# Performance work log

Hardware: AMD Instinct MI355X
Metric: run time of the kernel (lower is better)

The kernel has to match this reference:

```python
import jax, jax.numpy as jnp
import numpy as np

B, T, D = 2, 1024, 1024
H, HKV = 16, 8
HD = D // H           # 64
NREP = H // HKV       # 2
NLAYERS = 3
MAXKV = T * NLAYERS   # 3072
EPS = 1e-5


def setup_inputs() -> dict:
    key = jax.random.key(0)
    ks = jax.random.split(key, 8)
    # rotary tables over full accumulated-KV range
    inv_freq = 1.0 / (10000.0 ** (jnp.arange(0, HD, 2, dtype=jnp.float32) / HD))  # (HD/2,)
    t = jnp.arange(MAXKV, dtype=jnp.float32)
    freqs = jnp.outer(t, inv_freq)  # (MAXKV, HD/2)
    return {
        "x": jax.random.normal(ks[0], (B, T, D), jnp.float32),
        "cos": jnp.cos(freqs),
        "sin": jnp.sin(freqs),
        "q_w": jax.random.normal(ks[1], (NLAYERS, D, D), jnp.float32) * 0.02,
        "k_w": jax.random.normal(ks[2], (NLAYERS, D // NREP, D), jnp.float32) * 0.02,
        "v_w": jax.random.normal(ks[3], (NLAYERS, D // NREP, D), jnp.float32) * 0.02,
        "ln_w": jnp.ones((NLAYERS, D), jnp.float32),
        "lam": jax.random.normal(ks[4], (NLAYERS,), jnp.float32) * 0.1,
        "out_w": jax.random.normal(ks[5], (D, D), jnp.float32) * 0.02,
        "final_ln_w": jnp.ones((D,), jnp.float32),
        "alpha": jnp.ones((1,), jnp.float32),
    }


def rmsnorm(x, w):
    return x * jax.lax.rsqrt(jnp.mean(x * x, axis=-1, keepdims=True) + EPS) * w


def rope(x, cos, sin):
    # x: (B, L, h, HD); cos/sin: (MAXKV, HD/2); flash_attn non-interleaved rotary
    L = x.shape[1]
    c = jnp.concatenate([cos[:L], cos[:L]], axis=-1)[None, :, None, :]
    s = jnp.concatenate([sin[:L], sin[:L]], axis=-1)[None, :, None, :]
    x1, x2 = jnp.split(x, 2, axis=-1)
    rot = jnp.concatenate([-x2, x1], axis=-1)
    return x * c + rot * s


def reference(x, cos, sin, q_w, k_w, v_w, ln_w, lam, out_w, final_ln_w, alpha):
    scale = HD ** -0.5
    # lambda weights: layernorm over sigmoid of the 3 scalars (biased var, eps=1e-5)
    s = jax.nn.sigmoid(lam)
    lw = (s - s.mean()) * jax.lax.rsqrt(s.var() + EPS)
    qidx = jnp.arange(T)
    k_list, v_list = [], []
    acc = jnp.zeros_like(x)
    for i in range(NLAYERS):
        q = (x @ q_w[i].T).reshape(B, T, H, HD)
        k = (x @ k_w[i].T).reshape(B, T, HKV, HD)
        v = (x @ v_w[i].T).reshape(B, T, HKV, HD)
        k_list.append(k)
        v_list.append(v)
        K = jnp.concatenate(k_list, axis=1)  # (B, L, HKV, HD), L=(i+1)*T
        V = jnp.concatenate(v_list, axis=1)
        L = K.shape[1]
        qr = rope(q, cos, sin)
        Kr = rope(K, cos, sin)  # whole buffer re-rotated each layer, as in original
        Kr = jnp.repeat(Kr, NREP, axis=2)  # GQA expand
        Vr = jnp.repeat(V, NREP, axis=2)
        scores = jnp.einsum('bqhd,bkhd->bhqk', qr, Kr) * scale
        # flash_attn causal=True with kv_len > q_len aligns bottom-right
        mask = jnp.arange(L)[None, :] <= (qidx + (L - T))[:, None]
        scores = jnp.where(mask[None, None], scores, -jnp.inf)
        attn = jax.nn.softmax(scores, axis=-1)
        o = jnp.einsum('bhqk,bkhd->bqhd', attn, Vr).reshape(B, T, D)
        acc = acc + rmsnorm(o, ln_w[i]) * lw[i]
    out = rmsnorm(acc + alpha * x, final_ln_w)
    return out @ out_w.T
```

## Files before the change

### kernel.cpp

```cpp
#include <hip/hip_runtime.h>
#include <type_traits>
#include <utility>

typedef unsigned short u16;
typedef unsigned int u32;
typedef short short8 __attribute__((ext_vector_type(8)));
typedef __bf16 bf16x8 __attribute__((ext_vector_type(8)));
typedef float floatx4 __attribute__((ext_vector_type(4)));

template <typename V, typename = void> struct MfmaTakes : std::false_type {};
template <typename V>
struct MfmaTakes<V, std::void_t<decltype(__builtin_amdgcn_mfma_f32_16x16x32_bf16(
    std::declval<V>(), std::declval<V>(), std::declval<floatx4>(), 0, 0, 0))>>
    : std::true_type {};

template <typename V>
__device__ __forceinline__ floatx4 mfma_impl(V a, V b, floatx4 c, std::true_type) {
  return __builtin_amdgcn_mfma_f32_16x16x32_bf16(a, b, c, 0, 0, 0);
}
template <typename V>
__device__ __forceinline__ floatx4 mfma_impl(V a, V b, floatx4 c, std::false_type) {
  return __builtin_amdgcn_mfma_f32_16x16x32_bf16(
      __builtin_bit_cast(bf16x8, a), __builtin_bit_cast(bf16x8, b), c, 0, 0, 0);
}
__device__ __forceinline__ floatx4 MFMA16(short8 a, short8 b, floatx4 c) {
  return mfma_impl<short8>(a, b, c, MfmaTakes<short8>{});
}

__device__ __forceinline__ u16 f2bf(float f) {
  union { float f; unsigned u; } x; x.f = f;
  unsigned r = (x.u + 0x7fffu + ((x.u >> 16) & 1u)) >> 16;
  return (u16)r;
}
__device__ __forceinline__ float bf2f(u16 v) {
  union { unsigned u; float f; } x; x.u = ((unsigned)v) << 16; return x.f;
}
__device__ __forceinline__ u32 packbf(float lo, float hi) {
  return (__float_as_uint(hi) & 0xffff0000u) | (__float_as_uint(lo) >> 16);
}
__device__ __forceinline__ u32 pack2bf(float lo, float hi) {
  return ((u32)f2bf(hi) << 16) | (u32)f2bf(lo);
}

#if defined(__has_builtin)
#if __has_builtin(__builtin_amdgcn_global_load_lds)
#define HAS_GLLDS 1
#endif
#endif
__device__ __forceinline__ void stage16(const u16* g, u16* lbase, int lane) {
#ifdef HAS_GLLDS
  __builtin_amdgcn_global_load_lds(
      (__attribute__((address_space(1))) void*)(g),
      (__attribute__((address_space(3))) void*)(lbase), 16, 0, 0);
#else
  *(uint4*)(lbase + lane * 8) = *(const uint4*)g;
#endif
}

__global__ __launch_bounds__(256) void prep_kernel(
    const float* __restrict__ x, const float* __restrict__ qw,
    const float* __restrict__ kw, const float* __restrict__ vw,
    const float* __restrict__ outw, const float* __restrict__ lam,
    u16* __restrict__ xb, u16* __restrict__ wcat, u16* __restrict__ outwb,
    float* __restrict__ lwbuf) {
  size_t gid = (size_t)blockIdx.x * 256 + threadIdx.x;
  if (gid == 0) {
    float s0 = 1.f / (1.f + expf(-lam[0]));
    float s1 = 1.f / (1.f + expf(-lam[1]));
    float s2 = 1.f / (1.f + expf(-lam[2]));
    float mean = (s0 + s1 + s2) * (1.f / 3.f);
    float d0 = s0 - mean, d1 = s1 - mean, d2 = s2 - mean;
    float var = (d0 * d0 + d1 * d1 + d2 * d2) * (1.f / 3.f);
    float r = rsqrtf(var + 1e-5f);
    lwbuf[0] = d0 * r; lwbuf[1] = d1 * r; lwbuf[2] = d2 * r;
  }
  if (gid < 524288) {
    float4 v = ((const float4*)x)[gid];
    ushort4 o; o.x = f2bf(v.x); o.y = f2bf(v.y); o.z = f2bf(v.z); o.w = f2bf(v.w);
    ((ushort4*)xb)[gid] = o;
    return;
  }
  size_t g2 = gid - 524288;
  if (g2 < 1572864) {
    int col4 = (int)(g2 & 255);
    int n = (int)(g2 >> 8);
    int layer = n >> 11, r = n & 2047;
    const float* srcrow;
    if (r < 1024) srcrow = qw + ((size_t)(layer * 1024 + r) << 10);
    else if (r < 1536) srcrow = kw + ((size_t)(layer * 512 + (r - 1024)) << 10);
    else srcrow = vw + ((size_t)(layer * 512 + (r - 1536)) << 10);
    float4 v = ((const float4*)srcrow)[col4];
    ushort4 o; o.x = f2bf(v.x); o.y = f2bf(v.y); o.z = f2bf(v.z); o.w = f2bf(v.w);
    ((ushort4*)wcat)[g2] = o;
    return;
  }
  size_t g3 = g2 - 1572864;
  if (g3 < 262144) {
    float4 v = ((const float4*)outw)[g3];
    ushort4 o; o.x = f2bf(v.x); o.y = f2bf(v.y); o.z = f2bf(v.z); o.w = f2bf(v.w);
    ((ushort4*)outwb)[g3] = o;
  }
}

__global__ __launch_bounds__(256) void gemm_qkv(
    const u16* __restrict__ A, const u16* __restrict__ Bw,
    const float* __restrict__ cosb, const float* __restrict__ sinb,
    u16* __restrict__ qr, u16* __restrict__ kr, u16* __restrict__ vt) {
  __shared__ u16 As[128][64];
  __shared__ u16 Bs[128][64];
  const unsigned flat = blockIdx.x;
  const int bm = (flat >> 3) & 15;
  const int bn = ((flat >> 7) << 3) + (flat & 7);
  const int tid = threadIdx.x;
  const int wave = tid >> 6, lane = tid & 63;
  const int quad = lane >> 4, l16 = lane & 15;
  const int wm = wave & 1, wn = wave >> 1;
  const int srow = lane >> 3, skc = (lane & 7) * 8;
  floatx4 acc[4][4];
#pragma unroll
  for (int i = 0; i < 4; i++)
#pragma unroll
    for (int j = 0; j < 4; j++) { acc[i][j][0] = 0.f; acc[i][j][1] = 0.f; acc[i][j][2] = 0.f; acc[i][j][3] = 0.f; }
  const u16* Abase = A + (size_t)(bm * 128) * 1024;
  const u16* Bbase = Bw + (size_t)(bn * 128) * 1024;
  for (int k0 = 0; k0 < 1024; k0 += 64) {
    __syncthreads();
#pragma unroll
    for (int i = 0; i < 4; i++) {
      int ch = wave * 4 + i;
      stage16(Abase + (size_t)(ch * 8 + srow) * 1024 + k0 + skc, &As[ch * 8][0], lane);
      stage16(Bbase + (size_t)(ch * 8 + srow) * 1024 + k0 + skc, &Bs[ch * 8][0], lane);
    }
    __syncthreads();
#pragma unroll
    for (int kf = 0; kf < 2; kf++) {
      short8 af[4], bf[4];
#pragma unroll
      for (int mi = 0; mi < 4; mi++)
        af[mi] = *(const short8*)(&As[wm * 64 + mi * 16 + l16][kf * 32 + quad * 8]);
#pragma unroll
      for (int ni = 0; ni < 4; ni++)
        bf[ni] = *(const short8*)(&Bs[wn * 64 + ni * 16 + l16][kf * 32 + quad * 8]);
#pragma unroll
      for (int mi = 0; mi < 4; mi++)
#pragma unroll
        for (int ni = 0; ni < 4; ni++)
          acc[mi][ni] = MFMA16(af[mi], bf[ni], acc[mi][ni]);
    }
  }
  const int f0 = bn * 128 + wn * 64;
  const int lay = f0 >> 11;
  const int r0 = f0 & 2047;
  const int mrow0 = bm * 128 + wm * 64;
  if (r0 < 1024) {
    const int h = r0 >> 6;
#pragma unroll
    for (int mi = 0; mi < 4; mi++)
#pragma unroll
      for (int rr = 0; rr < 4; rr++) {
        int m = mrow0 + mi * 16 + quad * 4 + rr;
        int b = m >> 10, t = m & 1023;
        const float* cp = cosb + (size_t)t * 32;
        const float* sp = sinb + (size_t)t * 32;
        float c0 = cp[l16], s0 = sp[l16];
        float c1 = cp[16 + l16], s1 = sp[16 + l16];
        float x10 = acc[mi][0][rr], x20 = acc[mi][2][rr];
        float x11 = acc[mi][1][rr], x21 = acc[mi][3][rr];
        u16* row = qr + ((((size_t)lay * 2 + b) * 16 + h) * 1024 + t) * 64;
        row[l16]      = f2bf((x10 * c0 - x20 * s0) * 0.125f);
        row[16 + l16] = f2bf((x11 * c1 - x21 * s1) * 0.125f);
        row[32 + l16] = f2bf((x20 * c0 + x10 * s0) * 0.125f);
        row[48 + l16] = f2bf((x21 * c1 + x11 * s1) * 0.125f);
      }
  } else if (r0 < 1536) {
    const int hk = (r0 - 1024) >> 6;
#pragma unroll
    for (int mi = 0; mi < 4; mi++)
#pragma unroll
      for (int rr = 0; rr < 4; rr++) {
        int m = mrow0 + mi * 16 + quad * 4 + rr;
        int b = m >> 10, t = m & 1023;
        int pos = lay * 1024 + t;
        const float* cp = cosb + (size_t)pos * 32;
        const float* sp = sinb + (size_t)pos * 32;
        float c0 = cp[l16], s0 = sp[l16];
        float c1 = cp[16 + l16], s1 = sp[16 + l16];
        float x10 = acc[mi][0][rr], x20 = acc[mi][2][rr];
        float x11 = acc[mi][1][rr], x21 = acc[mi][3][rr];
        u16* row = kr + (((size_t)(b * 8 + hk)) * 3072 + pos) * 64;
        row[l16]      = f2bf(x10 * c0 - x20 * s0);
        row[16 + l16] = f2bf(x11 * c1 - x21 * s1);
        row[32 + l16] = f2bf(x20 * c0 + x10 * s0);
        row[48 + l16] = f2bf(x21 * c1 + x11 * s1);
      }
  } else {
    const int hv = (r0 - 1536) >> 6;
#pragma unroll
    for (int mi = 0; mi < 4; mi++) {
      int m0 = mrow0 + mi * 16 + quad * 4;
      int b = m0 >> 10;
      int pos0 = lay * 1024 + (m0 & 1023);
      u16* colbase = vt + ((size_t)(b * 8 + hv) * 64) * 3072 + pos0;
#pragma unroll
      for (int ni = 0; ni < 4; ni++) {
        int d = ni * 16 + l16;
        uint2 st;
        st.x = pack2bf(acc[mi][ni][0], acc[mi][ni][1]);
        st.y = pack2bf(acc[mi][ni][2], acc[mi][ni][3]);
        *(uint2*)(colbase + (size_t)d * 3072) = st;
      }
    }
  }
}

__global__ __launch_bounds__(256) void gemm_bt(
    const u16* __restrict__ A, const u16* __restrict__ Bw,
    float* __restrict__ C, int N, int K) {
  __shared__ u16 As[64][72];
  __shared__ u16 Bs[64][72];
  const int bm = blockIdx.x, bn = blockIdx.y;
  const int tid = threadIdx.x;
  const int wave = tid >> 6, lane = tid & 63;
  const int quad = lane >> 4, l16 = lane & 15;
  const int lr = tid >> 2, lc = (tid & 3) << 4;
  floatx4 acc[4];
#pragma unroll
  for (int i = 0; i < 4; i++) { acc[i][0] = 0.f; acc[i][1] = 0.f; acc[i][2] = 0.f; acc[i][3] = 0.f; }
  const u16* Arow = A + (size_t)(bm * 64 + lr) * K;
  const u16* Brow = Bw + (size_t)(bn * 64 + lr) * K;
  for (int k0 = 0; k0 < K; k0 += 64) {
    __syncthreads();
    *(uint4*)(&As[lr][lc])     = *(const uint4*)(Arow + k0 + lc);
    *(uint4*)(&As[lr][lc + 8]) = *(const uint4*)(Arow + k0 + lc + 8);
    *(uint4*)(&Bs[lr][lc])     = *(const uint4*)(Brow + k0 + lc);
    *(uint4*)(&Bs[lr][lc + 8]) = *(const uint4*)(Brow + k0 + lc + 8);
    __syncthreads();
    const int mrow = wave * 16 + l16;
    short8 a0 = *(const short8*)(&As[mrow][quad * 8]);
    short8 a1 = *(const short8*)(&As[mrow][32 + quad * 8]);
#pragma unroll
    for (int ns = 0; ns < 4; ns++) {
      short8 b0 = *(const short8*)(&Bs[ns * 16 + l16][quad * 8]);
      short8 b1 = *(const short8*)(&Bs[ns * 16 + l16][32 + quad * 8]);
      acc[ns] = MFMA16(a0, b0, acc[ns]);
      acc[ns] = MFMA16(a1, b1, acc[ns]);
    }
  }
#pragma unroll
  for (int ns = 0; ns < 4; ns++)
#pragma unroll
    for (int r = 0; r < 4; r++) {
      int row = bm * 64 + wave * 16 + quad * 4 + r;
      int col = bn * 64 + ns * 16 + l16;
      C[(size_t)row * N + col] = acc[ns][r];
    }
}

__global__ __launch_bounds__(256) void attn_v5(
    const u16* __restrict__ qr, const u16* __restrict__ kr,
    const u16* __restrict__ vt, u16* __restrict__ obS,
    float* __restrict__ lbufp) {
  __shared__ u16 Kt[32][72];
  __shared__ u16 Vtt[64][40];
  __shared__ u16 Pw[4][16][40];
  const unsigned flat = blockIdx.x;
  const int bhz = (int)((flat >> 6) * 8 + (flat & 7));
  const int qtile = 7 - (int)((flat >> 3) & 7);
  const int z = bhz >> 5;
  const int bh = bhz & 31;
  const int lay = (z == 5) ? 0 : ((z == 0 || z == 4) ? 1 : 2);
  const int n = lay * 32 + qtile * 4 + 4;
  int kt0, kt1;
  if (lay == 0) { kt0 = 0; kt1 = n; }
  else if (lay == 1) { int hf = n >> 1; kt0 = (z == 0) ? 0 : hf; kt1 = (z == 0) ? hf : n; }
  else {
    int t1 = n / 3, t2 = (2 * n) / 3;
    kt0 = (z == 1) ? 0 : ((z == 2) ? t1 : t2);
    kt1 = (z == 1) ? t1 : ((z == 2) ? t2 : n);
  }
  const int maskkt = lay * 32 + qtile * 4;
  const int b = bh >> 4, h = bh & 15, hk = h >> 1;
  const int tid = threadIdx.x, wave = tid >> 6, lane = tid & 63;
  const int quad = lane >> 4, l16 = lane & 15;
  const int qeffbase = lay * 1024 + qtile * 128 + wave * 32;
  const u16* qpb = qr + ((((size_t)lay * 2 + b) * 16 + h) * 1024
                         + qtile * 128 + wave * 32 + l16) * 64 + quad * 8;
  short8 qf[2][2];
  qf[0][0] = *(const short8*)(qpb);
  qf[0][1] = *(const short8*)(qpb + 32);
  qf[1][0] = *(const short8*)(qpb + 1024);
  qf[1][1] = *(const short8*)(qpb + 1056);
  const short8 ones = {16256, 16256, 16256, 16256, 16256, 16256, 16256, 16256};
  floatx4 oacc[2][4];
#pragma unroll
  for (int nt = 0; nt < 2; nt++)
#pragma unroll
    for (int dt = 0; dt < 4; dt++) { oacc[nt][dt][0] = 0.f; oacc[nt][dt][1] = 0.f; oacc[nt][dt][2] = 0.f; oacc[nt][dt][3] = 0.f; }
  floatx4 lacc[2];
  lacc[0][0] = 0.f; lacc[0][1] = 0.f; lacc[0][2] = 0.f; lacc[0][3] = 0.f;
  lacc[1] = lacc[0];
  const int ksr = tid >> 3, ksc = (tid & 7) * 8;
  const int vdr = tid >> 2, vdc = (tid & 3) * 8;
  const u16* kp = kr + ((size_t)(b * 8 + hk) * 3072 + kt0 * 32 + ksr) * 64 + ksc;
  const u16* vp = vt + ((size_t)(b * 8 + hk) * 64 + vdr) * 3072 + kt0 * 32 + vdc;
  uint4 kA = *(const uint4*)kp;
  uint4 vA = *(const uint4*)vp;
  for (int kt = kt0; kt < kt1; kt++) {
    kp += 2048; vp += 32;
    __syncthreads();
    *(uint4*)(&Kt[ksr][ksc])  = kA;
    *(uint4*)(&Vtt[vdr][vdc]) = vA;
    if (kt + 1 < kt1) { kA = *(const uint4*)kp; vA = *(const uint4*)vp; }
    __syncthreads();
    const bool needmask = (kt >= maskkt);
    uint2 pk[2][2];
#pragma unroll
    for (int mt = 0; mt < 2; mt++) {
      short8 kfa = *(const short8*)(&Kt[mt * 16 + l16][quad * 8]);
      short8 kfb = *(const short8*)(&Kt[mt * 16 + l16][32 + quad * 8]);
      const int keyb = kt * 32 + mt * 16 + quad * 4;
#pragma unroll
      for (int nt = 0; nt < 2; nt++) {
        floatx4 s; s[0] = 0.f; s[1] = 0.f; s[2] = 0.f; s[3] = 0.f;
        s = MFMA16(kfa, qf[nt][0], s);
        s = MFMA16(kfb, qf[nt][1], s);
        float p0 = __expf(s[0]), p1 = __expf(s[1]);
        float p2 = __expf(s[2]), p3 = __expf(s[3]);
        if (needmask) {
          int qpos = qeffbase + nt * 16 + l16;
          if (keyb + 0 > qpos) p0 = 0.f;
          if (keyb + 1 > qpos) p1 = 0.f;
          if (keyb + 2 > qpos) p2 = 0.f;
          if (keyb + 3 > qpos) p3 = 0.f;
        }
        pk[mt][nt].x = packbf(p0, p1);
        pk[mt][nt].y = packbf(p2, p3);
      }
    }
    short8 vf[4];
#pragma unroll
    for (int dt = 0; dt < 4; dt++)
      vf[dt] = *(const short8*)(&Vtt[dt * 16 + l16][quad * 8]);
#pragma unroll
    for (int nt = 0; nt < 2; nt++) {
      *(uint2*)(&Pw[wave][l16][quad * 4])      = pk[0][nt];
      *(uint2*)(&Pw[wave][l16][16 + quad * 4]) = pk[1][nt];
      short8 pf = *(const short8*)(&Pw[wave][l16][quad * 8]);
      lacc[nt] = MFMA16(ones, pf, lacc[nt]);
#pragma unroll
      for (int dt = 0; dt < 4; dt++)
        oacc[nt][dt] = MFMA16(vf[dt], pf, oacc[nt][dt]);
    }
  }
  float* Pf = (float*)(&Pw[wave][0][0]);
  const int tt = lane >> 2, dd = (lane & 3) << 2;
#pragma unroll
  for (int nt = 0; nt < 2; nt++) {
    int t = qtile * 128 + wave * 32 + nt * 16 + l16;
    if (quad == 0)
      lbufp[((size_t)z * 2048 + b * 1024 + t) * 16 + h] = lacc[nt][0];
    int t2 = qtile * 128 + wave * 32 + nt * 16 + tt;
    u16* orow = obS + ((size_t)(z * 2 + b) * 1024 + t2) * 1024 + h * 64 + dd;
#pragma unroll
    for (int dt = 0; dt < 4; dt++) {
      *(floatx4*)(&Pf[l16 * 20 + quad * 4]) = oacc[nt][dt];
      floatx4 val = *(const floatx4*)(&Pf[tt * 20 + dd]);
      uint2 st; st.x = pack2bf(val[0], val[1]); st.y = pack2bf(val[2], val[3]);
      *(uint2*)(orow + dt * 16) = st;
    }
  }
}

__device__ __forceinline__ float block_sum(float v, float* red) {
  v += __shfl_xor(v, 32); v += __shfl_xor(v, 16); v += __shfl_xor(v, 8);
  v += __shfl_xor(v, 4);  v += __shfl_xor(v, 2);  v += __shfl_xor(v, 1);
  __syncthreads();
  if ((threadIdx.x & 63) == 0) red[threadIdx.x >> 6] = v;
  __syncthreads();
  return red[0] + red[1] + red[2] + red[3];
}

__global__ __launch_bounds__(256) void fused_norm(
    const u16* __restrict__ obS, const float* __restrict__ lbufp,
    const float* __restrict__ x, const float* __restrict__ lnw,
    const float* __restrict__ lwbuf, const float* __restrict__ flnw,
    const float* __restrict__ alphap, u16* __restrict__ y) {
  __shared__ float red[4];
  const int row = blockIdx.x, tid = threadIdx.x;
  float a[4] = {0.f, 0.f, 0.f, 0.f};
  const int nsl[3] = {1, 2, 3};
  const int sl[3][3] = {{5, 0, 0}, {0, 4, 0}, {1, 2, 3}};
#pragma unroll
  for (int l = 0; l < 3; l++) {
    float o0 = 0.f, o1 = 0.f, o2 = 0.f, o3 = 0.f, ls = 0.f;
#pragma unroll
    for (int si = 0; si < 3; si++) {
      if (si >= nsl[l]) break;
      int z = sl[l][si];
      uint2 v = ((const uint2*)(obS + ((size_t)z * 2048 + row) * 1024))[tid];
      o0 += bf2f((u16)(v.x & 0xffff)); o1 += bf2f((u16)(v.x >> 16));
      o2 += bf2f((u16)(v.y & 0xffff)); o3 += bf2f((u16)(v.y >> 16));
      ls += lbufp[((size_t)z * 2048 + row) * 16 + (tid >> 4)];
    }
    float linv = 1.f / ls;
    float v0 = o0 * linv, v1 = o1 * linv, v2 = o2 * linv, v3 = o3 * linv;
    float ss = v0 * v0 + v1 * v1 + v2 * v2 + v3 * v3;
    ss = block_sum(ss, red);
    float rstd = rsqrtf(ss * (1.f / 1024.f) + 1e-5f);
    float lw = lwbuf[l];
    float4 w = ((const float4*)(lnw + (size_t)l * 1024))[tid];
    a[0] += v0 * rstd * w.x * lw;
    a[1] += v1 * rstd * w.y * lw;
    a[2] += v2 * rstd * w.z * lw;
    a[3] += v3 * rstd * w.w * lw;
  }
  const float aa = alphap[0];
  float4 xv = ((const float4*)(x + (size_t)row * 1024))[tid];
  float v0 = a[0] + aa * xv.x, v1 = a[1] + aa * xv.y;
  float v2 = a[2] + aa * xv.z, v3 = a[3] + aa * xv.w;
  float ss = v0 * v0 + v1 * v1 + v2 * v2 + v3 * v3;
  ss = block_sum(ss, red);
  float rstd = rsqrtf(ss * (1.f / 1024.f) + 1e-5f);
  float4 fw = ((const float4*)flnw)[tid];
  ushort4 o;
  o.x = f2bf(v0 * rstd * fw.x); o.y = f2bf(v1 * rstd * fw.y);
  o.z = f2bf(v2 * rstd * fw.z); o.w = f2bf(v3 * rstd * fw.w);
  ((ushort4*)(y + (size_t)row * 1024))[tid] = o;
}

extern "C" void kernel_launch(void* const* d_in, const int* in_sizes, int n_in,
                              void* d_out, int out_size, void* d_ws, size_t ws_size,
                              hipStream_t stream) {
  const float* x     = (const float*)d_in[0];
  const float* cosb  = (const float*)d_in[1];
  const float* sinb  = (const float*)d_in[2];
  const float* qw    = (const float*)d_in[3];
  const float* kw    = (const float*)d_in[4];
  const float* vw    = (const float*)d_in[5];
  const float* lnw   = (const float*)d_in[6];
  const float* lam   = (const float*)d_in[7];
  const float* outw  = (const float*)d_in[8];
  const float* flnw  = (const float*)d_in[9];
  const float* alphap= (const float*)d_in[10];
  float* out = (float*)d_out;
  char* ws = (char*)d_ws;
  u16*   xb    = (u16*)  (ws + 0);
  u16*   wcat  = (u16*)  (ws + 4194304);
  u16*   obS   = (u16*)  (ws + 0);
  u16*   outwb = (u16*)  (ws + 25165824);
  float* lwbuf = (float*)(ws + 27262976);
  u16*   qr    = (u16*)  (ws + 27264000);
  u16*   kr    = (u16*)  (ws + 39846912);
  u16*   vt    = (u16*)  (ws + 46138368);
  float* lbufp = (float*)(ws + 52429824);
  u16*   yb    = (u16*)  (ws + 53216256);

  prep_kernel<<<9216, 256, 0, stream>>>(x, qw, kw, vw, outw, lam, xb, wcat, outwb, lwbuf);
  gemm_qkv<<<768, 256, 0, stream>>>(xb, wcat, cosb, sinb, qr, kr, vt);
  attn_v5<<<1536, 256, 0, stream>>>(qr, kr, vt, obS, lbufp);
  fused_norm<<<2048, 256, 0, stream>>>(obS, lbufp, x, lnw, lwbuf, flnw, alphap, yb);
  gemm_bt<<<dim3(32, 16), 256, 0, stream>>>(yb, outwb, out, 1024, 1024);
}
```

Before: 253.9 us.

## Double-buffer attention K/V tiles, keep P in registers via 16x16x16 MFMA, use exp2

The attention kernel now double-buffers the K and V shared-memory tiles, which removes one of the two barriers per key tile. The P matrix no longer round-trips through shared memory; it feeds 16x16x16 bf16 MFMAs straight from registers. Q is prescaled by log2(e)/8 so the softmax exponent can use the hardware exp2. In exchange, the narrower MFMA needs twice as many instructions for PV and the row-sum, and shared-memory use for K/V doubles.

```diff
diff --git a/kernel.cpp b/kernel.cpp
--- a/kernel.cpp
+++ b/kernel.cpp
@@ -5,6 +5,7 @@
 typedef unsigned short u16;
 typedef unsigned int u32;
 typedef short short8 __attribute__((ext_vector_type(8)));
+typedef short s16x4 __attribute__((ext_vector_type(4)));
 typedef __bf16 bf16x8 __attribute__((ext_vector_type(8)));
 typedef float floatx4 __attribute__((ext_vector_type(4)));
 
@@ -26,6 +27,20 @@
 __device__ __forceinline__ floatx4 MFMA16(short8 a, short8 b, floatx4 c) {
   return mfma_impl<short8>(a, b, c, MfmaTakes<short8>{});
 }
+
+__device__ __forceinline__ floatx4 MFMAK16(s16x4 a, s16x4 b, floatx4 c) {
+  return __builtin_amdgcn_mfma_f32_16x16x16bf16_1k(a, b, c, 0, 0, 0);
+}
+
+#if defined(__has_builtin)
+#if __has_builtin(__builtin_amdgcn_exp2f)
+#define EXP2(x) __builtin_amdgcn_exp2f(x)
+#else
+#define EXP2(x) exp2f(x)
+#endif
+#else
+#define EXP2(x) exp2f(x)
+#endif
 
 __device__ __forceinline__ u16 f2bf(float f) {
   union { float f; unsigned u; } x; x.f = f;
@@ -56,6 +71,8 @@
   *(uint4*)(lbase + lane * 8) = *(const uint4*)g;
 #endif
 }
+
+#define QSCALE 0.18033688011112042f
 
 __global__ __launch_bounds__(256) void prep_kernel(
     const float* __restrict__ x, const float* __restrict__ qw,
@@ -167,10 +184,10 @@
         float x10 = acc[mi][0][rr], x20 = acc[mi][2][rr];
         float x11 = acc[mi][1][rr], x21 = acc[mi][3][rr];
         u16* row = qr + ((((size_t)lay * 2 + b) * 16 + h) * 1024 + t) * 64;
-        row[l16]      = f2bf((x10 * c0 - x20 * s0) * 0.125f);
-        row[16 + l16] = f2bf((x11 * c1 - x21 * s1) * 0.125f);
-        row[32 + l16] = f2bf((x20 * c0 + x10 * s0) * 0.125f);
-        row[48 + l16] = f2bf((x21 * c1 + x11 * s1) * 0.125f);
+        row[l16]      = f2bf((x10 * c0 - x20 * s0) * QSCALE);
+        row[16 + l16] = f2bf((x11 * c1 - x21 * s1) * QSCALE);
+        row[32 + l16] = f2bf((x20 * c0 + x10 * s0) * QSCALE);
+        row[48 + l16] = f2bf((x21 * c1 + x11 * s1) * QSCALE);
       }
   } else if (r0 < 1536) {
     const int hk = (r0 - 1024) >> 6;
@@ -256,13 +273,13 @@
     }
 }
 
-__global__ __launch_bounds__(256) void attn_v5(
+__global__ __launch_bounds__(256) void attn_v6(
     const u16* __restrict__ qr, const u16* __restrict__ kr,
     const u16* __restrict__ vt, u16* __restrict__ obS,
     float* __restrict__ lbufp) {
-  __shared__ u16 Kt[32][72];
-  __shared__ u16 Vtt[64][40];
-  __shared__ u16 Pw[4][16][40];
+  __shared__ __align__(16) u16 Kt[2][32][72];
+  __shared__ __align__(16) u16 Vtt[2][64][40];
+  __shared__ __align__(16) u16 Pw[4][16][40];
   const unsigned flat = blockIdx.x;
   const int bhz = (int)((flat >> 6) * 8 + (flat & 7));
   const int qtile = 7 - (int)((flat >> 3) & 7);
@@ -290,7 +307,7 @@
   qf[0][1] = *(const short8*)(qpb + 32);
   qf[1][0] = *(const short8*)(qpb + 1024);
   qf[1][1] = *(const short8*)(qpb + 1056);
-  const short8 ones = {16256, 16256, 16256, 16256, 16256, 16256, 16256, 16256};
+  const s16x4 ones4 = {16256, 16256, 16256, 16256};
   floatx4 oacc[2][4];
 #pragma unroll
   for (int nt = 0; nt < 2; nt++)
@@ -305,27 +322,33 @@
   const u16* vp = vt + ((size_t)(b * 8 + hk) * 64 + vdr) * 3072 + kt0 * 32 + vdc;
   uint4 kA = *(const uint4*)kp;
   uint4 vA = *(const uint4*)vp;
+  *(uint4*)(&Kt[0][ksr][ksc])  = kA;
+  *(uint4*)(&Vtt[0][vdr][vdc]) = vA;
+  kp += 2048; vp += 32;
+  if (kt0 + 1 < kt1) { kA = *(const uint4*)kp; vA = *(const uint4*)vp; }
   for (int kt = kt0; kt < kt1; kt++) {
-    kp += 2048; vp += 32;
+    const int p = (kt - kt0) & 1;
     __syncthreads();
-    *(uint4*)(&Kt[ksr][ksc])  = kA;
-    *(uint4*)(&Vtt[vdr][vdc]) = vA;
-    if (kt + 1 < kt1) { kA = *(const uint4*)kp; vA = *(const uint4*)vp; }
-    __syncthreads();
+    if (kt + 1 < kt1) {
+      *(uint4*)(&Kt[p ^ 1][ksr][ksc])  = kA;
+      *(uint4*)(&Vtt[p ^ 1][vdr][vdc]) = vA;
+      kp += 2048; vp += 32;
+      if (kt + 2 < kt1) { kA = *(const uint4*)kp; vA = *(const uint4*)vp; }
+    }
     const bool needmask = (kt >= maskkt);
     uint2 pk[2][2];
 #pragma unroll
     for (int mt = 0; mt < 2; mt++) {
-      short8 kfa = *(const short8*)(&Kt[mt * 16 + l16][quad * 8]);
-      short8 kfb = *(const short8*)(&Kt[mt * 16 + l16][32 + quad * 8]);
+      short8 kfa = *(const short8*)(&Kt[p][mt * 16 + l16][quad * 8]);
+      short8 kfb = *(const short8*)(&Kt[p][mt * 16 + l16][32 + quad * 8]);
       const int keyb = kt * 32 + mt * 16 + quad * 4;
 #pragma unroll
       for (int nt = 0; nt < 2; nt++) {
         floatx4 s; s[0] = 0.f; s[1] = 0.f; s[2] = 0.f; s[3] = 0.f;
         s = MFMA16(kfa, qf[nt][0], s);
         s = MFMA16(kfb, qf[nt][1], s);
-        float p0 = __expf(s[0]), p1 = __expf(s[1]);
-        float p2 = __expf(s[2]), p3 = __expf(s[3]);
+        float p0 = EXP2(s[0]), p1 = EXP2(s[1]);
+        float p2 = EXP2(s[2]), p3 = EXP2(s[3]);
         if (needmask) {
           int qpos = qeffbase + nt * 16 + l16;
           if (keyb + 0 > qpos) p0 = 0.f;
@@ -337,19 +360,23 @@
         pk[mt][nt].y = packbf(p2, p3);
       }
     }
-    short8 vf[4];
-#pragma unroll
-    for (int dt = 0; dt < 4; dt++)
-      vf[dt] = *(const short8*)(&Vtt[dt * 16 + l16][quad * 8]);
+    s16x4 vfr[2][4];
+#pragma unroll
+    for (int dt = 0; dt < 4; dt++) {
+      vfr[0][dt] = *(const s16x4*)(&Vtt[p][dt * 16 + l16][quad * 4]);
+      vfr[1][dt] = *(const s16x4*)(&Vtt[p][dt * 16 + l16][16 + quad * 4]);
+    }
 #pragma unroll
     for (int nt = 0; nt < 2; nt++) {
-      *(uint2*)(&Pw[wave][l16][quad * 4])      = pk[0][nt];
-      *(uint2*)(&Pw[wave][l16][16 + quad * 4]) = pk[1][nt];
-      short8 pf = *(const short8*)(&Pw[wave][l16][quad * 8]);
-      lacc[nt] = MFMA16(ones, pf, lacc[nt]);
-#pragma unroll
-      for (int dt = 0; dt < 4; dt++)
-        oacc[nt][dt] = MFMA16(vf[dt], pf, oacc[nt][dt]);
+      s16x4 p0f = __builtin_bit_cast(s16x4, pk[0][nt]);
+      s16x4 p1f = __builtin_bit_cast(s16x4, pk[1][nt]);
+      lacc[nt] = MFMAK16(ones4, p0f, lacc[nt]);
+      lacc[nt] = MFMAK16(ones4, p1f, lacc[nt]);
+#pragma unroll
+      for (int dt = 0; dt < 4; dt++) {
+        oacc[nt][dt] = MFMAK16(vfr[0][dt], p0f, oacc[nt][dt]);
+        oacc[nt][dt] = MFMAK16(vfr[1][dt], p1f, oacc[nt][dt]);
+      }
     }
   }
   float* Pf = (float*)(&Pw[wave][0][0]);
@@ -457,7 +484,7 @@
 
   prep_kernel<<<9216, 256, 0, stream>>>(x, qw, kw, vw, outw, lam, xb, wcat, outwb, lwbuf);
   gemm_qkv<<<768, 256, 0, stream>>>(xb, wcat, cosb, sinb, qr, kr, vt);
-  attn_v5<<<1536, 256, 0, stream>>>(qr, kr, vt, obS, lbufp);
+  attn_v6<<<1536, 256, 0, stream>>>(qr, kr, vt, obS, lbufp);
   fused_norm<<<2048, 256, 0, stream>>>(obS, lbufp, x, lnw, lwbuf, flnw, alphap, yb);
   gemm_bt<<<dim3(32, 16), 256, 0, stream>>>(yb, outwb, out, 1024, 1024);
 }
```

Result: no change. 254.5 us (+0.2%).
